# Optimization experiments

Measured on AMD Instinct MI355X. Metric: run time of the kernel, lower is better.

Reference implementation:

```python
import jax, jax.numpy as jnp
import numpy as np

B, L, S, D, H, TOPK = 8, 2048, 1000, 1024, 8, 10
E = D // H  # d_keys = 128


def setup_inputs() -> dict:
    key = jax.random.key(0)
    ks = jax.random.split(key, 8)
    s = 1.0 / np.sqrt(D)
    return {
        "target_embedding": jax.random.normal(ks[0], (B, L, D), dtype=jnp.float32),
        "source_embedding": jax.random.normal(ks[1], (S, D), dtype=jnp.float32),
        "Wq": jax.random.normal(ks[2], (D, D), dtype=jnp.float32) * s,
        "bq": jnp.zeros((D,), dtype=jnp.float32),
        "Wk": jax.random.normal(ks[3], (D, D), dtype=jnp.float32) * s,
        "bk": jnp.zeros((D,), dtype=jnp.float32),
        "Wo": jax.random.normal(ks[4], (D, D), dtype=jnp.float32) * s,
        "bo": jnp.zeros((D,), dtype=jnp.float32),
        "data_id": 0,
    }


def reference(target_embedding, source_embedding, Wq, bq, Wk, bk, Wo, bo, data_id):
    # data_id is unused by the original module's math.
    b, l, d = target_embedding.shape
    h, e, topk = H, E, TOPK
    scale = 1.0 / np.sqrt(e)

    q = (target_embedding @ Wq + bq).reshape(b, l, h, e)   # [B,L,H,E]
    k = (source_embedding @ Wk + bk).reshape(-1, h, e)      # [S,H,E]

    scores = jnp.einsum('blhe,she->bhls', q, k)             # [B,H,L,S]
    A = jax.nn.softmax(scale * scores, axis=-1)             # dropout is eval-mode identity
    tmps = A.sum(axis=2)                                    # [B,H,S] head-wise column mass
    _, idxs = jax.lax.top_k(tmps, topk)                     # [B,H,topk]

    kh = jnp.transpose(k, (1, 0, 2))                        # [H,S,E]
    # gather per (batch, head) the topk source key vectors
    tok = kh[jnp.arange(h)[None, :, None], idxs, :]         # [B,H,topk,E]
    tok = jnp.transpose(tok, (0, 2, 1, 3)).reshape(b, topk, h * e)  # [B,topk,D]
    return tok @ Wo + bo                                    # [B,topk,D]
```

## Files before the change

kernel.cpp:

```cpp
#include <hip/hip_runtime.h>
#include <hip/hip_bf16.h>
#include <math.h>

constexpr int B_ = 8;
constexpr int L_ = 2048;
constexpr int S_ = 1000;
constexpr int D_ = 1024;
constexpr int H_ = 8;
constexpr int E_ = 128;
constexpr int TOPK_ = 10;
constexpr float SCALE_LOG2E_ = 0.12751744f;

typedef __attribute__((ext_vector_type(8))) short short8;
typedef __attribute__((ext_vector_type(4))) float f32x4;

__device__ inline unsigned short f2bf(float x) {
    unsigned u = __float_as_uint(x);
    unsigned r = (u + 0x7fffu + ((u >> 16) & 1u)) >> 16;
    return (unsigned short)r;
}
__device__ inline float bf2f(unsigned short s) {
    return __uint_as_float(((unsigned)s) << 16);
}

__device__ __forceinline__ float fexp2(float x) {
#if __has_builtin(__builtin_amdgcn_exp2f)
    return __builtin_amdgcn_exp2f(x);
#else
    return __expf(x * 0.69314718056f);
#endif
}

typedef __attribute__((address_space(1))) const unsigned int gas_u32;
typedef __attribute__((address_space(3))) unsigned int las_u32;
__device__ __forceinline__ void gload_lds16(const void* g, void* l) {
    __builtin_amdgcn_global_load_lds((gas_u32*)g, (las_u32*)l, 16, 0, 0);
}

__global__ __launch_bounds__(256) void gemm_gather_bias_kernel(
    const float* __restrict__ Kbuf, const int* __restrict__ idxs,
    const float* __restrict__ Bm, const float* __restrict__ bias,
    float* __restrict__ C, int M, int N)
{
    __shared__ float As[16][65];
    __shared__ float Bs[16][68];

    const int t  = threadIdx.x;
    const int tx = t & 15;
    const int ty = t >> 4;
    const int m0 = blockIdx.y * 64;
    const int n0 = blockIdx.x * 64;

    float acc[4][4];
#pragma unroll
    for (int i = 0; i < 4; ++i)
#pragma unroll
        for (int j = 0; j < 4; ++j) acc[i][j] = 0.f;

    for (int k0 = 0; k0 < D_; k0 += 16) {
        {
            const int row = m0 + (t >> 2);
            const int k   = k0 + (t & 3) * 4;
            float4 v = {0.f, 0.f, 0.f, 0.f};
            if (row < M) {
                int b  = row / TOPK_;
                int tt = row - b * TOPK_;
                int s  = idxs[(b * H_ + (k >> 7)) * TOPK_ + tt];
                v = *(const float4*)&Kbuf[(size_t)s * D_ + k];
            }
            const int rr = t >> 2, c4 = (t & 3) * 4;
            As[c4 + 0][rr] = v.x;
            As[c4 + 1][rr] = v.y;
            As[c4 + 2][rr] = v.z;
            As[c4 + 3][rr] = v.w;
        }
        {
            const int row = t >> 4;
            const int c4  = (t & 15) * 4;
            float4 v = *(const float4*)&Bm[(size_t)(k0 + row) * N + n0 + c4];
            *(float4*)&Bs[row][c4] = v;
        }
        __syncthreads();
#pragma unroll
        for (int k = 0; k < 16; ++k) {
            float a[4], b[4];
#pragma unroll
            for (int i = 0; i < 4; ++i) a[i] = As[k][ty * 4 + i];
            float4 bv = *(const float4*)&Bs[k][tx * 4];
            b[0] = bv.x; b[1] = bv.y; b[2] = bv.z; b[3] = bv.w;
#pragma unroll
            for (int i = 0; i < 4; ++i)
#pragma unroll
                for (int j = 0; j < 4; ++j) acc[i][j] += a[i] * b[j];
        }
        __syncthreads();
    }

#pragma unroll
    for (int i = 0; i < 4; ++i) {
        const int row = m0 + ty * 4 + i;
        if (row < M) {
#pragma unroll
            for (int j = 0; j < 4; ++j) {
                const int col = n0 + tx * 4 + j;
                C[(size_t)row * N + col] = acc[i][j] + bias[col];
            }
        }
    }
}

__global__ __launch_bounds__(256) void splitWT2_kernel(
    const float* __restrict__ Wq, const float* __restrict__ Wk,
    unsigned short* __restrict__ WqTh, unsigned short* __restrict__ WqTl,
    unsigned short* __restrict__ WkTh, unsigned short* __restrict__ WkTl)
{
    const float* W = (blockIdx.z == 0) ? Wq : Wk;
    unsigned short* WTh = (blockIdx.z == 0) ? WqTh : WkTh;
    unsigned short* WTl = (blockIdx.z == 0) ? WqTl : WkTl;

    __shared__ __attribute__((aligned(16))) float tile[64][68];
    const int t  = threadIdx.x;
    const int k0 = blockIdx.y * 64, n0 = blockIdx.x * 64;
#pragma unroll
    for (int it = 0; it < 4; ++it) {
        int id = it * 256 + t;
        int r = id >> 4, c = id & 15;
        *(float4*)&tile[r][c * 4] = *(const float4*)&W[(size_t)(k0 + r) * D_ + n0 + c * 4];
    }
    __syncthreads();
#pragma unroll
    for (int it = 0; it < 4; ++it) {
        int id = it * 256 + t;
        int n = id >> 4, c = id & 15;
        unsigned short hs[4], ls[4];
#pragma unroll
        for (int i = 0; i < 4; ++i) {
            float x = tile[c * 4 + i][n];
            hs[i] = f2bf(x);
            ls[i] = f2bf(x - bf2f(hs[i]));
        }
        size_t o = (size_t)(n0 + n) * D_ + k0 + c * 4;
        uint2 uh; uh.x = (unsigned)hs[0] | ((unsigned)hs[1] << 16);
                  uh.y = (unsigned)hs[2] | ((unsigned)hs[3] << 16);
        uint2 ul; ul.x = (unsigned)ls[0] | ((unsigned)ls[1] << 16);
                  ul.y = (unsigned)ls[2] | ((unsigned)ls[3] << 16);
        *(uint2*)&WTh[o] = uh;
        *(uint2*)&WTl[o] = ul;
    }
}

__global__ __launch_bounds__(256, 2) void kproj_kernel(
    const float* __restrict__ src,
    const unsigned short* __restrict__ WkTh, const unsigned short* __restrict__ WkTl,
    const float* __restrict__ bk,
    float* __restrict__ Kbuf,
    unsigned short* __restrict__ Kh, unsigned short* __restrict__ Kl)
{
    __shared__ __attribute__((aligned(16))) unsigned short Bh[128 * 64];
    __shared__ __attribute__((aligned(16))) unsigned short Bl[128 * 64];

    const int t    = threadIdx.x;
    const int lane = t & 63, w = t >> 6;
    const int mb   = blockIdx.x >> 3;
    const int n0   = (blockIdx.x & 7) * 128;

    f32x4 acc[2][8];
#pragma unroll
    for (int m = 0; m < 2; ++m)
#pragma unroll
        for (int n = 0; n < 8; ++n) acc[m][n] = (f32x4){0.f, 0.f, 0.f, 0.f};

    for (int k0 = 0; k0 < D_; k0 += 64) {
        __syncthreads();
#pragma unroll
        for (int it = 0; it < 4; ++it) {
            int r = it * 32 + (t >> 3), c = t & 7;
            size_t gofs = (size_t)r * D_ + k0 + ((c ^ (r & 7)) << 3);
            int db = it * 4096 + t * 16;
            gload_lds16(&WkTh[(size_t)n0 * D_ + gofs], (char*)Bh + db);
            gload_lds16(&WkTl[(size_t)n0 * D_ + gofs], (char*)Bl + db);
        }
        __syncthreads();

#pragma unroll
        for (int ki = 0; ki < 2; ++ki) {
            short8 ah[2], al[2];
#pragma unroll
            for (int m = 0; m < 2; ++m) {
                int r = mb * 128 + w * 32 + m * 16 + (lane & 15);
                float4 x0 = {0.f, 0.f, 0.f, 0.f}, x1 = {0.f, 0.f, 0.f, 0.f};
                if (r < S_) {
                    const float* ga = &src[(size_t)r * D_ + k0 + (ki * 4 + (lane >> 4)) * 8];
                    x0 = *(const float4*)ga;
                    x1 = *(const float4*)(ga + 4);
                }
                float xs[8] = {x0.x, x0.y, x0.z, x0.w, x1.x, x1.y, x1.z, x1.w};
#pragma unroll
                for (int j = 0; j < 8; ++j) {
                    unsigned short hh = f2bf(xs[j]);
                    ah[m][j] = (short)hh;
                    al[m][j] = (short)f2bf(xs[j] - bf2f(hh));
                }
            }
#pragma unroll
            for (int n = 0; n < 8; ++n) {
                int nn = n * 16 + (lane & 15);
                int slot = ki * 4 + (lane >> 4);
                int lofs = nn * 64 + ((slot ^ (nn & 7)) << 3);
                short8 bh = *(short8*)&Bh[lofs];
                short8 bl = *(short8*)&Bl[lofs];
#pragma unroll
                for (int m = 0; m < 2; ++m) {
                    acc[m][n] = __builtin_amdgcn_mfma_f32_16x16x32_bf16(ah[m], bh, acc[m][n], 0, 0, 0);
                    acc[m][n] = __builtin_amdgcn_mfma_f32_16x16x32_bf16(ah[m], bl, acc[m][n], 0, 0, 0);
                    acc[m][n] = __builtin_amdgcn_mfma_f32_16x16x32_bf16(al[m], bh, acc[m][n], 0, 0, 0);
                }
            }
        }
    }

#pragma unroll
    for (int n = 0; n < 8; ++n) {
        int col = n0 + n * 16 + (lane & 15);
        float bkv = bk[col];
#pragma unroll
        for (int m = 0; m < 2; ++m) {
            int rbase = mb * 128 + w * 32 + m * 16 + ((lane >> 4) << 2);
#pragma unroll
            for (int r = 0; r < 4; ++r) {
                int row = rbase + r;
                unsigned short hh = 0, ll = 0;
                if (row < S_) {
                    float kv = acc[m][n][r] + bkv;
                    Kbuf[(size_t)row * D_ + col] = kv;
                    hh = f2bf(kv);
                    ll = f2bf(kv - bf2f(hh));
                }
                Kh[(size_t)row * D_ + col] = hh;
                Kl[(size_t)row * D_ + col] = ll;
            }
        }
    }
}

__global__ __launch_bounds__(256, 3) void qproj_kernel(
    const float* __restrict__ tgt,
    const unsigned short* __restrict__ WqTh, const unsigned short* __restrict__ WqTl,
    const float* __restrict__ bq,
    unsigned short* __restrict__ qhb, unsigned short* __restrict__ qlb)
{
    __shared__ __attribute__((aligned(16))) unsigned short Bh[2][128 * 32];
    __shared__ __attribute__((aligned(16))) unsigned short Bl[2][128 * 32];

    const int t    = threadIdx.x;
    const int lane = t & 63, w = t >> 6;
    const int x    = blockIdx.x & 7;
    const int jj   = blockIdx.x >> 3;
    const int n0   = (jj & 7) * 128;
    const int mb   = (jj >> 3) * 8 + x;

    f32x4 acc[2][8];
#pragma unroll
    for (int m = 0; m < 2; ++m)
#pragma unroll
        for (int n = 0; n < 8; ++n) acc[m][n] = (f32x4){0.f, 0.f, 0.f, 0.f};

#define QB_ISSUE(KT, BUF)                                                   \
    do {                                                                    \
        _Pragma("unroll")                                                   \
        for (int it = 0; it < 2; ++it) {                                    \
            int id = it * 256 + t;                                          \
            int line = id >> 4, sub = id & 15;                              \
            int gs = sub ^ (line & 15);                                     \
            size_t gb = (size_t)(n0 + line * 4 + (gs >> 2)) * D_            \
                        + (KT) * 32 + ((gs & 3) << 3);                      \
            gload_lds16(&WqTh[gb], (char*)&Bh[(BUF)][0] + id * 16);         \
            gload_lds16(&WqTl[gb], (char*)&Bl[(BUF)][0] + id * 16);         \
        }                                                                   \
    } while (0)

#define QA_LOAD(KT, XA)                                                     \
    do {                                                                    \
        _Pragma("unroll")                                                   \
        for (int m = 0; m < 2; ++m) {                                       \
            int r = mb * 128 + w * 32 + m * 16 + (lane & 15);               \
            const float* ga = &tgt[(size_t)r * D_ + (KT) * 32 + (lane >> 4) * 8]; \
            XA[m][0] = *(const float4*)ga;                                  \
            XA[m][1] = *(const float4*)(ga + 4);                            \
        }                                                                   \
    } while (0)

#define QP_COMPUTE(XA, BUF)                                                 \
    do {                                                                    \
        short8 ah[2], al[2];                                                \
        _Pragma("unroll")                                                   \
        for (int m = 0; m < 2; ++m) {                                       \
            float xs[8] = {XA[m][0].x, XA[m][0].y, XA[m][0].z, XA[m][0].w,  \
                           XA[m][1].x, XA[m][1].y, XA[m][1].z, XA[m][1].w}; \
            _Pragma("unroll")                                               \
            for (int j = 0; j < 8; ++j) {                                   \
                unsigned short hh = f2bf(xs[j]);                            \
                ah[m][j] = (short)hh;                                       \
                al[m][j] = (short)f2bf(xs[j] - bf2f(hh));                   \
            }                                                               \
        }                                                                   \
        _Pragma("unroll")                                                   \
        for (int n = 0; n < 8; ++n) {                                       \
            int nn   = n * 16 + (lane & 15);                                \
            int line = nn >> 2;                                             \
            int sub  = (nn & 3) * 4 + (lane >> 4);                          \
            int lofs = line * 128 + ((sub ^ (line & 15)) << 3);             \
            short8 bh = *(short8*)&Bh[(BUF)][lofs];                         \
            short8 bl = *(short8*)&Bl[(BUF)][lofs];                         \
            _Pragma("unroll")                                               \
            for (int m = 0; m < 2; ++m) {                                   \
                acc[m][n] = __builtin_amdgcn_mfma_f32_16x16x32_bf16(ah[m], bh, acc[m][n], 0, 0, 0); \
                acc[m][n] = __builtin_amdgcn_mfma_f32_16x16x32_bf16(ah[m], bl, acc[m][n], 0, 0, 0); \
                acc[m][n] = __builtin_amdgcn_mfma_f32_16x16x32_bf16(al[m], bh, acc[m][n], 0, 0, 0); \
            }                                                               \
        }                                                                   \
    } while (0)

    float4 xa0[2][2], xa1[2][2];
    QB_ISSUE(0, 0);
    QA_LOAD(0, xa0);

#pragma unroll 1
    for (int kt2 = 0; kt2 < 16; ++kt2) {
        const int kt = kt2 * 2;
        __syncthreads();
        if (kt + 1 < 32) { QB_ISSUE(kt + 1, 1); QA_LOAD(kt + 1, xa1); }
        QP_COMPUTE(xa0, 0);
        __syncthreads();
        if (kt + 2 < 32) { QB_ISSUE(kt + 2, 0); QA_LOAD(kt + 2, xa0); }
        QP_COMPUTE(xa1, 1);
    }
#undef QB_ISSUE
#undef QA_LOAD
#undef QP_COMPUTE

#pragma unroll
    for (int n = 0; n < 8; ++n) {
        int col = n0 + n * 16 + (lane & 15);
        float bqv = bq[col];
#pragma unroll
        for (int m = 0; m < 2; ++m) {
            int rbase = mb * 128 + w * 32 + m * 16 + ((lane >> 4) << 2);
#pragma unroll
            for (int r = 0; r < 4; ++r) {
                float q = (acc[m][n][r] + bqv) * SCALE_LOG2E_;
                unsigned short hh = f2bf(q);
                qhb[(size_t)(rbase + r) * D_ + col] = hh;
                qlb[(size_t)(rbase + r) * D_ + col] = f2bf(q - bf2f(hh));
            }
        }
    }
}

__global__ __launch_bounds__(256, 2) void scores2p_kernel(
    const unsigned short* __restrict__ qhb, const unsigned short* __restrict__ qlb,
    const unsigned short* __restrict__ Kh, const unsigned short* __restrict__ Kl,
    float* __restrict__ tmps, int b0)
{
    __shared__ __attribute__((aligned(16))) unsigned short KB[2][4][32 * 128];
    __shared__ float tmps_l[1024];

    const int t    = threadIdx.x;
    const int lane = t & 63, w = t >> 6;
    const int blk  = blockIdx.x;
    const int bb   = blk >> 6;
    const int h    = (blk >> 3) & 7;
    const int lt   = blk & 7;
    const int qrow0 = bb * L_ + lt * 256;
    const int bh_i  = (b0 + bb) * H_ + h;
    const int kr0   = t >> 4;
    const int kc0   = t & 15;

    for (int i = t; i < 1024; i += 256) tmps_l[i] = 0.f;

#define SC_ISSUE0(ST, BUF)                                                  \
    do {                                                                    \
        _Pragma("unroll")                                                   \
        for (int it = 0; it < 4; ++it) {                                    \
            int r = it * 16 + kr0;                                          \
            size_t g = (size_t)((ST) * 64 + r) * D_ + h * E_                \
                       + ((kc0 ^ (r & 15)) << 3);                           \
            int db = (it & 1) * 4096 + t * 16;                              \
            gload_lds16(&Kh[g], (char*)&KB[(BUF)][it >> 1][0] + db);        \
        }                                                                   \
    } while (0)

#define SC_ISSUE1(ST, BUF)                                                  \
    do {                                                                    \
        _Pragma("unroll")                                                   \
        for (int it = 0; it < 4; ++it) {                                    \
            int r = it * 16 + kr0;                                          \
            size_t g = (size_t)((ST) * 64 + r) * D_ + h * E_                \
                       + ((kc0 ^ (r & 15)) << 3);                           \
            int pl = it >> 1;                                               \
            int db = (it & 1) * 4096 + t * 16;                              \
            gload_lds16(&Kh[g], (char*)&KB[(BUF)][pl][0] + db);             \
            gload_lds16(&Kl[g], (char*)&KB[(BUF)][pl + 2][0] + db);         \
        }                                                                   \
    } while (0)

    SC_ISSUE0(0, 1);

    short8 qh[4][4], ql[4][4];
#pragma unroll
    for (int ch = 0; ch < 8; ++ch) {
        __syncthreads();
#pragma unroll
        for (int it = 0; it < 2; ++it) {
            int r = it * 16 + kr0;
            size_t g = (size_t)(qrow0 + ch * 32 + r) * D_ + h * E_ + kc0 * 8;
            int lofs = r * 128 + ((kc0 ^ (r & 15)) << 3);
            *(uint4*)&KB[0][0][lofs] = *(const uint4*)&qhb[g];
            *(uint4*)&KB[0][1][lofs] = *(const uint4*)&qlb[g];
        }
        __syncthreads();
        if ((ch >> 1) == w) {
#pragma unroll
            for (int j = 0; j < 2; ++j) {
                int rg = (ch & 1) * 2 + j;
#pragma unroll
                for (int ki = 0; ki < 4; ++ki) {
                    int rq = j * 16 + (lane & 15);
                    int slot = ki * 4 + (lane >> 4);
                    int lofs = rq * 128 + ((slot ^ (rq & 15)) << 3);
                    qh[rg][ki] = *(short8*)&KB[0][0][lofs];
                    ql[rg][ki] = *(short8*)&KB[0][1][lofs];
                }
            }
        }
    }

    float zacc[4][4];
#pragma unroll
    for (int rg = 0; rg < 4; ++rg)
#pragma unroll
        for (int r = 0; r < 4; ++r) zacc[rg][r] = 0.f;
    float invZ[4][4];

    int cur = 1;

    for (int u = 0; u < 16; ++u) {
        __syncthreads();
        if (u < 15) SC_ISSUE0(u + 1, cur ^ 1);
        else        SC_ISSUE1(0, cur ^ 1);

#pragma unroll
        for (int nfh = 0; nfh < 2; ++nfh) {
            f32x4 acc[4][2];
#pragma unroll
            for (int rg = 0; rg < 4; ++rg)
#pragma unroll
                for (int n2 = 0; n2 < 2; ++n2) acc[rg][n2] = (f32x4){0.f, 0.f, 0.f, 0.f};

#pragma unroll
            for (int ki = 0; ki < 4; ++ki)
#pragma unroll
                for (int n2 = 0; n2 < 2; ++n2) {
                    int nf = nfh * 2 + n2;
                    int sr = nf * 16 + (lane & 15);
                    int slot = ki * 4 + (lane >> 4);
                    int lofs = (sr & 31) * 128 + ((slot ^ (sr & 15)) << 3);
                    short8 bh = *(short8*)&KB[cur][sr >> 5][lofs];
#pragma unroll
                    for (int rg = 0; rg < 4; ++rg)
                        acc[rg][n2] = __builtin_amdgcn_mfma_f32_16x16x32_bf16(qh[rg][ki], bh, acc[rg][n2], 0, 0, 0);
                }

#pragma unroll
            for (int n2 = 0; n2 < 2; ++n2) {
                int s = u * 64 + (nfh * 2 + n2) * 16 + (lane & 15);
                if (s < S_) {
#pragma unroll
                    for (int rg = 0; rg < 4; ++rg)
#pragma unroll
                        for (int r = 0; r < 4; ++r)
                            zacc[rg][r] += fexp2(acc[rg][n2][r]);
                }
            }
        }

        if (u == 15) {
#pragma unroll
            for (int rg = 0; rg < 4; ++rg)
#pragma unroll
                for (int r = 0; r < 4; ++r) {
                    float z = zacc[rg][r];
                    z += __shfl_xor(z, 1);
                    z += __shfl_xor(z, 2);
                    z += __shfl_xor(z, 4);
                    z += __shfl_xor(z, 8);
                    invZ[rg][r] = 1.f / z;
                }
        }
        cur ^= 1;
    }

    for (int u = 0; u < 16; ++u) {
        __syncthreads();
        if (u < 15) SC_ISSUE1(u + 1, cur ^ 1);

#pragma unroll
        for (int nfh = 0; nfh < 2; ++nfh) {
            f32x4 acc[4][2];
#pragma unroll
            for (int rg = 0; rg < 4; ++rg)
#pragma unroll
                for (int n2 = 0; n2 < 2; ++n2) acc[rg][n2] = (f32x4){0.f, 0.f, 0.f, 0.f};

#pragma unroll
            for (int ki = 0; ki < 4; ++ki)
#pragma unroll
                for (int n2 = 0; n2 < 2; ++n2) {
                    int nf = nfh * 2 + n2;
                    int sr = nf * 16 + (lane & 15);
                    int pl = sr >> 5;
                    int slot = ki * 4 + (lane >> 4);
                    int lofs = (sr & 31) * 128 + ((slot ^ (sr & 15)) << 3);
                    short8 bh = *(short8*)&KB[cur][pl][lofs];
                    short8 bl = *(short8*)&KB[cur][pl + 2][lofs];
#pragma unroll
                    for (int rg = 0; rg < 4; ++rg) {
                        acc[rg][n2] = __builtin_amdgcn_mfma_f32_16x16x32_bf16(qh[rg][ki], bh, acc[rg][n2], 0, 0, 0);
                        acc[rg][n2] = __builtin_amdgcn_mfma_f32_16x16x32_bf16(qh[rg][ki], bl, acc[rg][n2], 0, 0, 0);
                        acc[rg][n2] = __builtin_amdgcn_mfma_f32_16x16x32_bf16(ql[rg][ki], bh, acc[rg][n2], 0, 0, 0);
                    }
                }

#pragma unroll
            for (int n2 = 0; n2 < 2; ++n2) {
                int s = u * 64 + (nfh * 2 + n2) * 16 + (lane & 15);
                if (s < S_) {
                    float val = 0.f;
#pragma unroll
                    for (int rg = 0; rg < 4; ++rg)
#pragma unroll
                        for (int r = 0; r < 4; ++r)
                            val += fexp2(acc[rg][n2][r]) * invZ[rg][r];
                    atomicAdd(&tmps_l[s], val);
                }
            }
        }
        cur ^= 1;
    }
#undef SC_ISSUE0
#undef SC_ISSUE1

    __syncthreads();
    for (int i = t; i < S_; i += 256)
        atomicAdd(&tmps[(size_t)bh_i * S_ + i], tmps_l[i]);
}

__global__ __launch_bounds__(256) void topk_kernel(
    const float* __restrict__ tmps, int* __restrict__ idxs)
{
    const int bh = blockIdx.x;
    const int t  = threadIdx.x;
    __shared__ float v[S_];
    __shared__ float rv[256];
    __shared__ int   ri[256];

    for (int i = t; i < S_; i += 256) v[i] = tmps[(size_t)bh * S_ + i];
    __syncthreads();

    for (int it = 0; it < TOPK_; ++it) {
        float best = -1e38f;
        int bi = 0x7fffffff;
        for (int s = t; s < S_; s += 256) {
            const float x = v[s];
            if (x > best) { best = x; bi = s; }
        }
        rv[t] = best; ri[t] = bi;
        __syncthreads();
        for (int k = 128; k > 0; k >>= 1) {
            if (t < k) {
                const float x = rv[t + k];
                const int  xi = ri[t + k];
                if (x > rv[t] || (x == rv[t] && xi < ri[t])) { rv[t] = x; ri[t] = xi; }
            }
            __syncthreads();
        }
        if (t == 0) {
            idxs[bh * TOPK_ + it] = ri[0];
            v[ri[0]] = -1e38f;
        }
        __syncthreads();
    }
}

extern "C" void kernel_launch(void* const* d_in, const int* in_sizes, int n_in,
                              void* d_out, int out_size, void* d_ws, size_t ws_size,
                              hipStream_t stream)
{
    const float* tgt = (const float*)d_in[0];
    const float* src = (const float*)d_in[1];
    const float* Wq  = (const float*)d_in[2];
    const float* bq  = (const float*)d_in[3];
    const float* Wk  = (const float*)d_in[4];
    const float* bk  = (const float*)d_in[5];
    const float* Wo  = (const float*)d_in[6];
    const float* bo  = (const float*)d_in[7];
    float* out = (float*)d_out;

    char* ws = (char*)d_ws;
    size_t off = 0;
    float*          Kbuf = (float*)(ws + off);          off += (size_t)S_ * D_ * 4;
    float*          tmps = (float*)(ws + off);          off += (size_t)B_ * H_ * S_ * 4;
    int*            idxs = (int*)(ws + off);            off += (size_t)B_ * H_ * TOPK_ * 4;
    off = (off + 255) & ~(size_t)255;
    unsigned short* Kh   = (unsigned short*)(ws + off); off += (size_t)1024 * D_ * 2;
    unsigned short* Kl   = (unsigned short*)(ws + off); off += (size_t)1024 * D_ * 2;
    unsigned short* WqTh = (unsigned short*)(ws + off); off += (size_t)D_ * D_ * 2;
    unsigned short* WqTl = (unsigned short*)(ws + off); off += (size_t)D_ * D_ * 2;
    unsigned short* WkTh = (unsigned short*)(ws + off); off += (size_t)D_ * D_ * 2;
    unsigned short* WkTl = (unsigned short*)(ws + off); off += (size_t)D_ * D_ * 2;
    unsigned short* planes = (unsigned short*)(ws + off);
    const size_t fixed_bytes = off;
    const size_t plane_elems_per_b = (size_t)L_ * D_;

    int nb_fit = 1;
    if (ws_size > fixed_bytes) {
        size_t f = (ws_size - fixed_bytes) / (2 * plane_elems_per_b * 2);
        nb_fit = (f < 1) ? 1 : (f > 8 ? 8 : (int)f);
    }

    hipMemsetAsync(tmps, 0, (size_t)B_ * H_ * S_ * sizeof(float), stream);

    {
        dim3 g(D_ / 64, D_ / 64, 2);
        splitWT2_kernel<<<g, 256, 0, stream>>>(Wq, Wk, WqTh, WqTl, WkTh, WkTl);
    }

    kproj_kernel<<<64, 256, 0, stream>>>(src, WkTh, WkTl, bk, Kbuf, Kh, Kl);

    for (int b0 = 0; b0 < B_; b0 += nb_fit) {
        int nb = (B_ - b0 < nb_fit) ? (B_ - b0) : nb_fit;
        unsigned short* qhb = planes;
        unsigned short* qlb = qhb + (size_t)nb_fit * plane_elems_per_b;

        qproj_kernel<<<nb * 128, 256, 0, stream>>>(
            tgt + (size_t)b0 * L_ * D_, WqTh, WqTl, bq, qhb, qlb);
        scores2p_kernel<<<nb * 64, 256, 0, stream>>>(qhb, qlb, Kh, Kl, tmps, b0);
    }

    topk_kernel<<<B_ * H_, 256, 0, stream>>>(tmps, idxs);

    {
        dim3 g(D_ / 64, (B_ * TOPK_ + 63) / 64);
        gemm_gather_bias_kernel<<<g, 256, 0, stream>>>(
            Kbuf, idxs, Wo, bo, out, B_ * TOPK_, D_);
    }
}
```

Baseline: 412.6 us.

## Double-buffer K projection tiles and prefetch next tile during MFMA compute

Rewrites the K-projection GEMM main loop to use two 32-wide k-tile LDS buffers. The next tile of the transposed Wk and the next source activations are loaded while MFMAs run on the current tile. This aims to hide global-to-LDS latency that the previous load-sync-compute loop exposed. The launch bound goes from 2 to 3 blocks per CU, which tightens register limits. The kernel also now runs twice as many barrier-separated steps.

```diff
diff --git a/kernel.cpp b/kernel.cpp
--- a/kernel.cpp
+++ b/kernel.cpp
@@ -149,15 +149,15 @@
     }
 }
 
-__global__ __launch_bounds__(256, 2) void kproj_kernel(
+__global__ __launch_bounds__(256, 3) void kproj_kernel(
     const float* __restrict__ src,
     const unsigned short* __restrict__ WkTh, const unsigned short* __restrict__ WkTl,
     const float* __restrict__ bk,
     float* __restrict__ Kbuf,
     unsigned short* __restrict__ Kh, unsigned short* __restrict__ Kl)
 {
-    __shared__ __attribute__((aligned(16))) unsigned short Bh[128 * 64];
-    __shared__ __attribute__((aligned(16))) unsigned short Bl[128 * 64];
+    __shared__ __attribute__((aligned(16))) unsigned short Bh[2][128 * 32];
+    __shared__ __attribute__((aligned(16))) unsigned short Bl[2][128 * 32];
 
     const int t    = threadIdx.x;
     const int lane = t & 63, w = t >> 6;
@@ -170,54 +170,84 @@
 #pragma unroll
         for (int n = 0; n < 8; ++n) acc[m][n] = (f32x4){0.f, 0.f, 0.f, 0.f};
 
-    for (int k0 = 0; k0 < D_; k0 += 64) {
-        __syncthreads();
-#pragma unroll
-        for (int it = 0; it < 4; ++it) {
-            int r = it * 32 + (t >> 3), c = t & 7;
-            size_t gofs = (size_t)r * D_ + k0 + ((c ^ (r & 7)) << 3);
-            int db = it * 4096 + t * 16;
-            gload_lds16(&WkTh[(size_t)n0 * D_ + gofs], (char*)Bh + db);
-            gload_lds16(&WkTl[(size_t)n0 * D_ + gofs], (char*)Bl + db);
-        }
-        __syncthreads();
-
-#pragma unroll
-        for (int ki = 0; ki < 2; ++ki) {
-            short8 ah[2], al[2];
-#pragma unroll
-            for (int m = 0; m < 2; ++m) {
-                int r = mb * 128 + w * 32 + m * 16 + (lane & 15);
-                float4 x0 = {0.f, 0.f, 0.f, 0.f}, x1 = {0.f, 0.f, 0.f, 0.f};
-                if (r < S_) {
-                    const float* ga = &src[(size_t)r * D_ + k0 + (ki * 4 + (lane >> 4)) * 8];
-                    x0 = *(const float4*)ga;
-                    x1 = *(const float4*)(ga + 4);
-                }
-                float xs[8] = {x0.x, x0.y, x0.z, x0.w, x1.x, x1.y, x1.z, x1.w};
-#pragma unroll
-                for (int j = 0; j < 8; ++j) {
-                    unsigned short hh = f2bf(xs[j]);
-                    ah[m][j] = (short)hh;
-                    al[m][j] = (short)f2bf(xs[j] - bf2f(hh));
-                }
-            }
-#pragma unroll
-            for (int n = 0; n < 8; ++n) {
-                int nn = n * 16 + (lane & 15);
-                int slot = ki * 4 + (lane >> 4);
-                int lofs = nn * 64 + ((slot ^ (nn & 7)) << 3);
-                short8 bh = *(short8*)&Bh[lofs];
-                short8 bl = *(short8*)&Bl[lofs];
-#pragma unroll
-                for (int m = 0; m < 2; ++m) {
-                    acc[m][n] = __builtin_amdgcn_mfma_f32_16x16x32_bf16(ah[m], bh, acc[m][n], 0, 0, 0);
-                    acc[m][n] = __builtin_amdgcn_mfma_f32_16x16x32_bf16(ah[m], bl, acc[m][n], 0, 0, 0);
-                    acc[m][n] = __builtin_amdgcn_mfma_f32_16x16x32_bf16(al[m], bh, acc[m][n], 0, 0, 0);
-                }
-            }
-        }
-    }
+#define KB_ISSUE(KT, BUF)                                                   \
+    do {                                                                    \
+        _Pragma("unroll")                                                   \
+        for (int it = 0; it < 2; ++it) {                                    \
+            int id = it * 256 + t;                                          \
+            int line = id >> 4, sub = id & 15;                              \
+            int gs = sub ^ (line & 15);                                     \
+            size_t gb = (size_t)(n0 + line * 4 + (gs >> 2)) * D_            \
+                        + (KT) * 32 + ((gs & 3) << 3);                      \
+            gload_lds16(&WkTh[gb], (char*)&Bh[(BUF)][0] + id * 16);         \
+            gload_lds16(&WkTl[gb], (char*)&Bl[(BUF)][0] + id * 16);         \
+        }                                                                   \
+    } while (0)
+
+#define KA_LOAD(KT, XA)                                                     \
+    do {                                                                    \
+        _Pragma("unroll")                                                   \
+        for (int m = 0; m < 2; ++m) {                                       \
+            int r = mb * 128 + w * 32 + m * 16 + (lane & 15);               \
+            if (r < S_) {                                                   \
+                const float* ga = &src[(size_t)r * D_ + (KT) * 32 + (lane >> 4) * 8]; \
+                XA[m][0] = *(const float4*)ga;                              \
+                XA[m][1] = *(const float4*)(ga + 4);                        \
+            } else {                                                        \
+                XA[m][0] = (float4){0.f, 0.f, 0.f, 0.f};                    \
+                XA[m][1] = (float4){0.f, 0.f, 0.f, 0.f};                    \
+            }                                                               \
+        }                                                                   \
+    } while (0)
+
+#define KP_COMPUTE(XA, BUF)                                                 \
+    do {                                                                    \
+        short8 ah[2], al[2];                                                \
+        _Pragma("unroll")                                                   \
+        for (int m = 0; m < 2; ++m) {                                       \
+            float xs[8] = {XA[m][0].x, XA[m][0].y, XA[m][0].z, XA[m][0].w,  \
+                           XA[m][1].x, XA[m][1].y, XA[m][1].z, XA[m][1].w}; \
+            _Pragma("unroll")                                               \
+            for (int j = 0; j < 8; ++j) {                                   \
+                unsigned short hh = f2bf(xs[j]);                            \
+                ah[m][j] = (short)hh;                                       \
+                al[m][j] = (short)f2bf(xs[j] - bf2f(hh));                   \
+            }                                                               \
+        }                                                                   \
+        _Pragma("unroll")                                                   \
+        for (int n = 0; n < 8; ++n) {                                       \
+            int nn   = n * 16 + (lane & 15);                                \
+            int line = nn >> 2;                                             \
+            int sub  = (nn & 3) * 4 + (lane >> 4);                          \
+            int lofs = line * 128 + ((sub ^ (line & 15)) << 3);             \
+            short8 bh = *(short8*)&Bh[(BUF)][lofs];                         \
+            short8 bl = *(short8*)&Bl[(BUF)][lofs];                         \
+            _Pragma("unroll")                                               \
+            for (int m = 0; m < 2; ++m) {                                   \
+                acc[m][n] = __builtin_amdgcn_mfma_f32_16x16x32_bf16(ah[m], bh, acc[m][n], 0, 0, 0); \
+                acc[m][n] = __builtin_amdgcn_mfma_f32_16x16x32_bf16(ah[m], bl, acc[m][n], 0, 0, 0); \
+                acc[m][n] = __builtin_amdgcn_mfma_f32_16x16x32_bf16(al[m], bh, acc[m][n], 0, 0, 0); \
+            }                                                               \
+        }                                                                   \
+    } while (0)
+
+    float4 xa0[2][2], xa1[2][2];
+    KB_ISSUE(0, 0);
+    KA_LOAD(0, xa0);
+
+#pragma unroll 1
+    for (int kt2 = 0; kt2 < 16; ++kt2) {
+        const int kt = kt2 * 2;
+        __syncthreads();
+        if (kt + 1 < 32) { KB_ISSUE(kt + 1, 1); KA_LOAD(kt + 1, xa1); }
+        KP_COMPUTE(xa0, 0);
+        __syncthreads();
+        if (kt + 2 < 32) { KB_ISSUE(kt + 2, 0); KA_LOAD(kt + 2, xa0); }
+        KP_COMPUTE(xa1, 1);
+    }
+#undef KB_ISSUE
+#undef KA_LOAD
+#undef KP_COMPUTE
 
 #pragma unroll
     for (int n = 0; n < 8; ++n) {
```

Result: no change. 417.4 us (+1.2%).
